# Performance work log

Hardware: AMD Instinct MI355X
Metric: run time of the kernel (lower is better)

Reference implementation:

```python
import jax, jax.numpy as jnp
import numpy as np

IN_F = 1024
OUT_F = 2048
BATCH = 1024
LAMBD = 0.2
TOL = 1e-4
MAX_ITERS = 100


def setup_inputs() -> dict:
    key = jax.random.key(0)
    kx, kw = jax.random.split(key)
    x = jax.random.normal(kx, (BATCH, IN_F), dtype=jnp.float32)
    # weight init exactly as in torch __init__: randn then column-wise (dim=0) L2 normalization
    w = jax.random.normal(kw, (OUT_F, IN_F), dtype=jnp.float32)
    w = w / jnp.linalg.norm(w, axis=0)  # norm over out_features, broadcast over columns
    A = w.T  # (in, out)
    M = A.T @ A + jnp.eye(OUT_F, dtype=jnp.float32)  # (out, out)
    M_inv = jnp.linalg.inv(M).T
    return {"x": x, "weight": w, "M_inv": M_inv}


def _softshrink(z, lambd):
    return jnp.sign(z) * jnp.maximum(jnp.abs(z) - lambd, 0.0)


def _basis_pursuit_admm(A_dot_b, M_inv, lambd=LAMBD, tol=TOL, max_iters=MAX_ITERS):
    # Mask-based equivalent of the torch dynamic-resizing loop: solved rows are
    # frozen instead of removed; v_solution captures v at the iteration a row converges.
    B, Mdim = A_dot_b.shape
    z = jnp.zeros((B, Mdim), dtype=A_dot_b.dtype)
    solved0 = jnp.zeros((B,), dtype=bool)
    init = (z, z, z, z, solved0)  # v, u, v_prev, v_solution, solved

    def step(carry, _):
        v, u, v_prev, v_sol, solved = carry
        b_eff = A_dot_b + v - u                      # (B, M)
        xk = b_eff @ M_inv                           # (B, M) @ (M, M)
        v_new = _softshrink(xk + u, lambd)
        u_new = u + xk - v_new
        # negligible_improvement on the updated v vs previous v
        dx = jnp.linalg.norm(v_new - v_prev, axis=1)
        xn = jnp.linalg.norm(v_new, axis=1)
        conv = (dx / xn) < tol
        newly = conv & (~solved)
        v_sol = jnp.where(newly[:, None], v_new, v_sol)
        frozen = solved[:, None]
        v = jnp.where(frozen, v, v_new)
        u = jnp.where(frozen, u, u_new)
        solved = solved | newly
        return (v, u, v, v_sol, solved), None

    (v, u, v_prev, v_sol, solved), _ = jax.lax.scan(step, init, None, length=max_iters)
    # Matches torch: rows still unsolved after max_iters keep their initial zero solution.
    return v_sol


def reference(x, weight, M_inv):
    input_shape = x.shape
    b = jax.lax.stop_gradient(x.reshape(x.shape[0], -1))  # x.detach() in torch
    A_dot_b = b @ weight.T                                 # b.matmul(A) with A = weight.T
    encoded = _basis_pursuit_admm(A_dot_b, M_inv)
    decoded = encoded @ weight
    return encoded, decoded.reshape(input_shape)
```

## Files before the change

### kernel.cpp

```cpp
#include <hip/hip_runtime.h>
#include <math.h>

#define BATCH 1024
#define IN_F  1024
#define OUT_F 2048
#define LAMBD 0.2f
#define TOL   1e-4f
#define MAX_ITERS 100

#define KSPLIT 4
#define KCHUNK (OUT_F / KSPLIT)
#define BSCALE 32.0f
#define BSCALE_INV 0.03125f

typedef _Float16 half8 __attribute__((ext_vector_type(8)));
typedef _Float16 half4 __attribute__((ext_vector_type(4)));
typedef float    floatx16 __attribute__((ext_vector_type(16)));
typedef unsigned char fp8_t;

#define GLOAD_LDS16(g, l) __builtin_amdgcn_global_load_lds(              \
    (const __attribute__((address_space(1))) void*)(g),                  \
    (__attribute__((address_space(3))) void*)(l), 16, 0, 0)

__device__ inline int pk4_fp8(float a, float b, float c, float d) {
    int w = __builtin_amdgcn_cvt_pk_fp8_f32(a, b, 0, false);
    w = __builtin_amdgcn_cvt_pk_fp8_f32(c, d, w, true);
    return w;
}
__device__ inline fp8_t enc_fp8(float a) {
    return (fp8_t)(__builtin_amdgcn_cvt_pk_fp8_f32(a, a, 0, false) & 0xff);
}
__device__ inline void cvt4_fp8(int w, float o[4]) {
    o[0] = __builtin_amdgcn_cvt_f32_fp8(w, 0);
    o[1] = __builtin_amdgcn_cvt_f32_fp8(w, 1);
    o[2] = __builtin_amdgcn_cvt_f32_fp8(w, 2);
    o[3] = __builtin_amdgcn_cvt_f32_fp8(w, 3);
}

__global__ void init_kernel(float4* __restrict__ v16, float4* __restrict__ u16,
                            float4* __restrict__ enc, int* __restrict__ solved) {
    const int i = blockIdx.x * blockDim.x + threadIdx.x;
    const float4 z = make_float4(0.f, 0.f, 0.f, 0.f);
    const int nh = BATCH * OUT_F / 8;
    const int n4 = BATCH * OUT_F / 4;
    if (i < nh) { v16[i] = z; u16[i] = z; }
    if (i < n4) enc[i] = z;
    if (i < BATCH) solved[i] = 0;
}

__global__ __launch_bounds__(256)
void cast_f16_kernel(const float* __restrict__ in, _Float16* __restrict__ out, int n) {
    const int i = (blockIdx.x * 256 + threadIdx.x) * 4;
    if (i < n) {
        const float4 f = *(const float4*)&in[i];
        half4 h;
        h[0] = (_Float16)f.x; h[1] = (_Float16)f.y;
        h[2] = (_Float16)f.z; h[3] = (_Float16)f.w;
        *(half4*)&out[i] = h;
    }
}

__global__ __launch_bounds__(256)
void transpose_w_kernel(const float* __restrict__ W, _Float16* __restrict__ WT) {
    __shared__ float tile[32][33];
    const int tid = threadIdx.x;
    const int row0 = blockIdx.y * 32;
    const int col0 = blockIdx.x * 32;
    const int r = tid >> 3;
    const int c4 = (tid & 7) * 4;
    const float4 b4 = *(const float4*)&W[(size_t)(row0 + r) * IN_F + col0 + c4];
    tile[r][c4 + 0] = b4.x; tile[r][c4 + 1] = b4.y;
    tile[r][c4 + 2] = b4.z; tile[r][c4 + 3] = b4.w;
    __syncthreads();
    half4 h;
#pragma unroll
    for (int j = 0; j < 4; ++j) h[j] = (_Float16)tile[c4 + j][r];
    *(half4*)&WT[(size_t)(col0 + r) * OUT_F + row0 + c4] = h;
}

__global__ __launch_bounds__(256)
void split_b_kernel(const float* __restrict__ B, fp8_t* __restrict__ BhT) {
    __shared__ float tile[32][33];
    const int tid = threadIdx.x;
    const int k0 = blockIdx.y * 32;
    const int n0 = blockIdx.x * 32;
    const int r = tid >> 3;
    const int c4 = (tid & 7) * 4;
    const float4 b4 = *(const float4*)&B[(size_t)(k0 + r) * OUT_F + n0 + c4];
    tile[r][c4 + 0] = b4.x; tile[r][c4 + 1] = b4.y;
    tile[r][c4 + 2] = b4.z; tile[r][c4 + 3] = b4.w;
    __syncthreads();
    const int w = pk4_fp8(tile[c4 + 0][r] * BSCALE, tile[c4 + 1][r] * BSCALE,
                          tile[c4 + 2][r] * BSCALE, tile[c4 + 3][r] * BSCALE);
    *(int*)&BhT[(size_t)(n0 + r) * OUT_F + k0 + c4] = w;
}

__global__ __launch_bounds__(256)
void mfma_nt_ab(const _Float16* __restrict__ A, const _Float16* __restrict__ B,
                _Float16* __restrict__ Abh, fp8_t* __restrict__ Ah,
                int N, int K) {
    __shared__ _Float16 sA[128 * 32];
    __shared__ _Float16 sB[128 * 32];
    const int tid = threadIdx.x;
    const int m0 = blockIdx.y * 128;
    const int n0 = blockIdx.x * 128;
    const int wv = tid >> 6, ln = tid & 63;
    const int half = ln >> 5, l31 = ln & 31;
    const int wm = (wv >> 1) * 64, wn = (wv & 1) * 64;
    const int r0 = tid >> 2, koff = (tid & 3) * 8;
    const size_t ga0 = (size_t)(m0 + r0) * K + koff;
    const size_t ga1 = (size_t)(m0 + r0 + 64) * K + koff;
    const size_t gb0 = (size_t)(n0 + r0) * K + koff;
    const size_t gb1 = (size_t)(n0 + r0 + 64) * K + koff;
    const int ldst0 = tid * 8, ldst1 = (256 + tid) * 8;

    floatx16 acc[2][2];
#pragma unroll
    for (int a = 0; a < 2; ++a)
#pragma unroll
        for (int b = 0; b < 2; ++b)
#pragma unroll
            for (int q = 0; q < 16; ++q) acc[a][b][q] = 0.f;

    for (int k = 0; k < K; k += 32) {
        __syncthreads();
        GLOAD_LDS16(A + ga0 + k, sA + ldst0);
        GLOAD_LDS16(A + ga1 + k, sA + ldst1);
        GLOAD_LDS16(B + gb0 + k, sB + ldst0);
        GLOAD_LDS16(B + gb1 + k, sB + ldst1);
        __syncthreads();
#pragma unroll
        for (int kk = 0; kk < 2; ++kk) {
            const int ko = kk * 16 + half * 8;
            const half8 a0 = *(const half8*)&sA[(wm + l31) * 32 + ko];
            const half8 a1 = *(const half8*)&sA[(wm + 32 + l31) * 32 + ko];
            const half8 b0 = *(const half8*)&sB[(wn + l31) * 32 + ko];
            const half8 b1 = *(const half8*)&sB[(wn + 32 + l31) * 32 + ko];
            acc[0][0] = __builtin_amdgcn_mfma_f32_32x32x16_f16(a0, b0, acc[0][0], 0, 0, 0);
            acc[0][1] = __builtin_amdgcn_mfma_f32_32x32x16_f16(a0, b1, acc[0][1], 0, 0, 0);
            acc[1][0] = __builtin_amdgcn_mfma_f32_32x32x16_f16(a1, b0, acc[1][0], 0, 0, 0);
            acc[1][1] = __builtin_amdgcn_mfma_f32_32x32x16_f16(a1, b1, acc[1][1], 0, 0, 0);
        }
    }
#pragma unroll
    for (int mm = 0; mm < 2; ++mm)
#pragma unroll
        for (int nn = 0; nn < 2; ++nn) {
            const int col = n0 + wn + nn * 32 + l31;
#pragma unroll
            for (int q = 0; q < 16; ++q) {
                const int row = m0 + wm + mm * 32 + (q & 3) + 8 * (q >> 2) + 4 * half;
                const size_t o = (size_t)row * N + col;
                const float x = acc[mm][nn][q];
                Abh[o] = (_Float16)x;
                Ah[o] = enc_fp8(x);
            }
        }
}

__global__ __launch_bounds__(256)
void mfma_nn_dec(const _Float16* __restrict__ A, const _Float16* __restrict__ B,
                 float* __restrict__ C, int N, int K) {
    __shared__ _Float16 sA[128 * 32];
    __shared__ _Float16 sB[128 * 32];
    const int tid = threadIdx.x;
    const int m0 = blockIdx.y * 128;
    const int n0 = blockIdx.x * 128;
    const int wv = tid >> 6, ln = tid & 63;
    const int half = ln >> 5, l31 = ln & 31;
    const int wm = (wv >> 1) * 64, wn = (wv & 1) * 64;
    const int r0 = tid >> 2, koff = (tid & 3) * 8;
    const size_t ga0 = (size_t)(m0 + r0) * K + koff;
    const size_t ga1 = (size_t)(m0 + r0 + 64) * K + koff;
    const size_t gb0 = (size_t)(n0 + r0) * K + koff;
    const size_t gb1 = (size_t)(n0 + r0 + 64) * K + koff;
    const int ldst0 = tid * 8, ldst1 = (256 + tid) * 8;

    floatx16 acc[2][2];
#pragma unroll
    for (int a = 0; a < 2; ++a)
#pragma unroll
        for (int b = 0; b < 2; ++b)
#pragma unroll
            for (int q = 0; q < 16; ++q) acc[a][b][q] = 0.f;

    for (int k = 0; k < K; k += 32) {
        __syncthreads();
        GLOAD_LDS16(A + ga0 + k, sA + ldst0);
        GLOAD_LDS16(A + ga1 + k, sA + ldst1);
        GLOAD_LDS16(B + gb0 + k, sB + ldst0);
        GLOAD_LDS16(B + gb1 + k, sB + ldst1);
        __syncthreads();
#pragma unroll
        for (int kk = 0; kk < 2; ++kk) {
            const int ko = kk * 16 + half * 8;
            const half8 a0 = *(const half8*)&sA[(wm + l31) * 32 + ko];
            const half8 a1 = *(const half8*)&sA[(wm + 32 + l31) * 32 + ko];
            const half8 b0 = *(const half8*)&sB[(wn + l31) * 32 + ko];
            const half8 b1 = *(const half8*)&sB[(wn + 32 + l31) * 32 + ko];
            acc[0][0] = __builtin_amdgcn_mfma_f32_32x32x16_f16(a0, b0, acc[0][0], 0, 0, 0);
            acc[0][1] = __builtin_amdgcn_mfma_f32_32x32x16_f16(a0, b1, acc[0][1], 0, 0, 0);
            acc[1][0] = __builtin_amdgcn_mfma_f32_32x32x16_f16(a1, b0, acc[1][0], 0, 0, 0);
            acc[1][1] = __builtin_amdgcn_mfma_f32_32x32x16_f16(a1, b1, acc[1][1], 0, 0, 0);
        }
    }
#pragma unroll
    for (int mm = 0; mm < 2; ++mm)
#pragma unroll
        for (int nn = 0; nn < 2; ++nn) {
            const int col = n0 + wn + nn * 32 + l31;
#pragma unroll
            for (int q = 0; q < 16; ++q) {
                const int row = m0 + wm + mm * 32 + (q & 3) + 8 * (q >> 2) + 4 * half;
                C[(size_t)row * N + col] = acc[mm][nn][q];
            }
        }
}

__global__ __launch_bounds__(256)
void xk_mfma(const fp8_t* __restrict__ Ah, const fp8_t* __restrict__ BhT,
             fp8_t* __restrict__ xkp, const int* __restrict__ solved) {
    __shared__ fp8_t smem[16384];
    fp8_t* sA = smem;
    fp8_t* sB = smem + 8192;
    const int tid = threadIdx.x;
    const int m0 = blockIdx.y * 128;
    const int n0 = blockIdx.x * 128;
    const int kz = blockIdx.z;
    constexpr size_t P = (size_t)BATCH * OUT_F;

    __shared__ int s_active;
    if (tid == 0) s_active = 0;
    __syncthreads();
    if (tid < 128 && solved[m0 + tid] == 0) s_active = 1;
    __syncthreads();
    if (!s_active) return;

    const int wv = tid >> 6;
    const int ln = tid & 63;
    const int half = ln >> 5;
    const int l31 = ln & 31;
    const int wm = (wv >> 1) * 64;
    const int wn = (wv & 1) * 64;

    const int r = tid & 127;
    const int c0 = tid >> 7;
    const fp8_t* gA = Ah  + (size_t)(m0 + r) * OUT_F + kz * KCHUNK;
    const fp8_t* gB = BhT + (size_t)(n0 + r) * OUT_F + kz * KCHUNK;
    fp8_t* lA0 = sA + (c0 * 128 + r) * 16;
    fp8_t* lA1 = sA + ((c0 + 2) * 128 + r) * 16;
    fp8_t* lB0 = sB + (c0 * 128 + r) * 16;
    fp8_t* lB1 = sB + ((c0 + 2) * 128 + r) * 16;

    floatx16 acc[2][2];
#pragma unroll
    for (int a = 0; a < 2; ++a)
#pragma unroll
        for (int b = 0; b < 2; ++b)
#pragma unroll
            for (int q = 0; q < 16; ++q) acc[a][b][q] = 0.f;

    const int ao0 = (wm + l31) * 16 + half * 8;
    const int ao1 = (wm + 32 + l31) * 16 + half * 8;
    const int bo0 = (wn + l31) * 16 + half * 8;
    const int bo1 = (wn + 32 + l31) * 16 + half * 8;

    for (int k = 0; k < KCHUNK; k += 64) {
        __syncthreads();
        GLOAD_LDS16(gA + k + c0 * 16, lA0);
        GLOAD_LDS16(gA + k + (c0 + 2) * 16, lA1);
        GLOAD_LDS16(gB + k + c0 * 16, lB0);
        GLOAD_LDS16(gB + k + (c0 + 2) * 16, lB1);
        __syncthreads();

#pragma unroll
        for (int kk = 0; kk < 4; ++kk) {
            const int cb = kk * 2048;
            const long long a0 = *(const long long*)&sA[cb + ao0];
            const long long a1 = *(const long long*)&sA[cb + ao1];
            const long long b0 = *(const long long*)&sB[cb + bo0];
            const long long b1 = *(const long long*)&sB[cb + bo1];
            acc[0][0] = __builtin_amdgcn_mfma_f32_32x32x16_fp8_fp8(a0, b0, acc[0][0], 0, 0, 0);
            acc[0][1] = __builtin_amdgcn_mfma_f32_32x32x16_fp8_fp8(a0, b1, acc[0][1], 0, 0, 0);
            acc[1][0] = __builtin_amdgcn_mfma_f32_32x32x16_fp8_fp8(a1, b0, acc[1][0], 0, 0, 0);
            acc[1][1] = __builtin_amdgcn_mfma_f32_32x32x16_fp8_fp8(a1, b1, acc[1][1], 0, 0, 0);
        }
    }

    __syncthreads();
#pragma unroll
    for (int mm = 0; mm < 2; ++mm)
#pragma unroll
        for (int nn = 0; nn < 2; ++nn) {
            const int lcol = wn + nn * 32 + l31;
#pragma unroll
            for (int q = 0; q < 16; ++q) {
                const int lrow = wm + mm * 32 + (q & 3) + 8 * (q >> 2) + 4 * half;
                smem[lrow * 128 + lcol] = enc_fp8(acc[mm][nn][q] * BSCALE_INV);
            }
        }
    __syncthreads();
    fp8_t* outp = xkp + kz * P + (size_t)m0 * OUT_F + n0;
#pragma unroll
    for (int s = 0; s < 4; ++s) {
        const int f = (s * 256 + tid) * 16;
        *(int4*)&outp[(size_t)(f >> 7) * OUT_F + (f & 127)] = *(const int4*)&smem[f];
    }
}

__global__ __launch_bounds__(256)
void update_kernel(const fp8_t* __restrict__ xkp, const _Float16* __restrict__ Abh,
                   _Float16* __restrict__ v, _Float16* __restrict__ u,
                   float* __restrict__ enc, fp8_t* __restrict__ Ah,
                   int* __restrict__ solved) {
    const int row = blockIdx.x;
    if (solved[row]) return;
    const int t = threadIdx.x;
    constexpr size_t P = (size_t)BATCH * OUT_F;

    const int c = t * 8;
    const size_t off = (size_t)row * OUT_F + c;
    const int2 q0 = *(const int2*)&xkp[off];
    const int2 q1 = *(const int2*)&xkp[P + off];
    const int2 q2 = *(const int2*)&xkp[2 * P + off];
    const int2 q3 = *(const int2*)&xkp[3 * P + off];
    const half8 u8 = *(const half8*)&u[off];
    const half8 v8 = *(const half8*)&v[off];
    const half8 ab8 = *(const half8*)&Abh[off];

    float f0[4], f1[4], f2[4], f3[4], g0[4], g1[4], g2[4], g3[4];
    cvt4_fp8(q0.x, f0); cvt4_fp8(q1.x, f1); cvt4_fp8(q2.x, f2); cvt4_fp8(q3.x, f3);
    cvt4_fp8(q0.y, g0); cvt4_fp8(q1.y, g1); cvt4_fp8(q2.y, g2); cvt4_fp8(q3.y, g3);
    float xs[8];
#pragma unroll
    for (int j = 0; j < 4; ++j) {
        xs[j] = f0[j] + f1[j] + f2[j] + f3[j];
        xs[j + 4] = g0[j] + g1[j] + g2[j] + g3[j];
    }

    float vn_all[8], ae[8];
    half8 vo, uo;
    float dx2 = 0.f, xn2 = 0.f;
#pragma unroll
    for (int j = 0; j < 8; ++j) {
        const float xk = xs[j];
        const float uv = (float)u8[j];
        const float vp = (float)v8[j];
        const float z = xk + uv;
        const float az = fabsf(z) - LAMBD;
        const float vnew = az > 0.f ? copysignf(az, z) : 0.f;
        const float unew = uv + xk - vnew;
        const float d = vnew - vp;
        dx2 += d * d;
        xn2 += vnew * vnew;
        vn_all[j] = vnew;
        vo[j] = (_Float16)vnew;
        uo[j] = (_Float16)unew;
        ae[j] = (float)ab8[j] + vnew - unew;
    }
    *(half8*)&v[off] = vo;
    *(half8*)&u[off] = uo;
    int2 ah;
    ah.x = pk4_fp8(ae[0], ae[1], ae[2], ae[3]);
    ah.y = pk4_fp8(ae[4], ae[5], ae[6], ae[7]);
    *(int2*)&Ah[off] = ah;

#pragma unroll
    for (int o = 32; o > 0; o >>= 1) {
        dx2 += __shfl_down(dx2, o);
        xn2 += __shfl_down(xn2, o);
    }
    __shared__ float sdx[4], sxn[4];
    __shared__ float s_conv;
    if ((t & 63) == 0) { sdx[t >> 6] = dx2; sxn[t >> 6] = xn2; }
    __syncthreads();
    if (t == 0) {
        const float dxt = sqrtf(sdx[0] + sdx[1] + sdx[2] + sdx[3]);
        const float xnt = sqrtf(sxn[0] + sxn[1] + sxn[2] + sxn[3]);
        const bool conv = (dxt / xnt) < TOL;
        s_conv = conv ? 1.f : 0.f;
        if (conv) solved[row] = 1;
    }
    __syncthreads();
    if (s_conv != 0.f) {
        *(float4*)&enc[off] = make_float4(vn_all[0], vn_all[1], vn_all[2], vn_all[3]);
        *(float4*)&enc[off + 4] = make_float4(vn_all[4], vn_all[5], vn_all[6], vn_all[7]);
    }
}

extern "C" void kernel_launch(void* const* d_in, const int* in_sizes, int n_in,
                              void* d_out, int out_size, void* d_ws, size_t ws_size,
                              hipStream_t stream) {
    (void)in_sizes; (void)n_in; (void)out_size; (void)ws_size;
    const float* x    = (const float*)d_in[0];
    const float* w    = (const float*)d_in[1];
    const float* Minv = (const float*)d_in[2];

    float* enc = (float*)d_out;
    float* dec = enc + (size_t)BATCH * OUT_F;

    constexpr size_t P = (size_t)BATCH * OUT_F;
    _Float16* Abh = (_Float16*)d_ws;
    _Float16* v   = Abh + P;
    _Float16* u   = v + P;
    _Float16* xh  = u + P;
    _Float16* wh  = xh + (size_t)BATCH * IN_F;
    _Float16* whT = wh + (size_t)OUT_F * IN_F;
    _Float16* ench = whT + (size_t)IN_F * OUT_F;
    fp8_t* Ah  = (fp8_t*)(ench + P);
    fp8_t* xkp = Ah + P;
    fp8_t* BhT = xkp + 4 * P;
    int* solved = (int*)(BhT + (size_t)OUT_F * OUT_F);

    {
        const int n = BATCH * OUT_F / 4;
        init_kernel<<<(n + 255) / 256, 256, 0, stream>>>(
            (float4*)v, (float4*)u, (float4*)enc, solved);
    }

    split_b_kernel<<<dim3(OUT_F / 32, OUT_F / 32), 256, 0, stream>>>(Minv, BhT);

    cast_f16_kernel<<<(BATCH * IN_F / 4 + 255) / 256, 256, 0, stream>>>(x, xh, BATCH * IN_F);
    cast_f16_kernel<<<(OUT_F * IN_F / 4 + 255) / 256, 256, 0, stream>>>(w, wh, OUT_F * IN_F);
    transpose_w_kernel<<<dim3(IN_F / 32, OUT_F / 32), 256, 0, stream>>>(w, whT);

    mfma_nt_ab<<<dim3(OUT_F / 128, BATCH / 128), 256, 0, stream>>>(
        xh, wh, Abh, Ah, OUT_F, IN_F);

    for (int it = 0; it < MAX_ITERS; ++it) {
        xk_mfma<<<dim3(OUT_F / 128, BATCH / 128, KSPLIT), 256, 0, stream>>>(
            Ah, BhT, xkp, solved);
        update_kernel<<<BATCH, 256, 0, stream>>>(xkp, Abh, v, u, enc, Ah, solved);
    }

    cast_f16_kernel<<<(BATCH * OUT_F / 4 + 255) / 256, 256, 0, stream>>>(enc, ench, BATCH * OUT_F);
    mfma_nn_dec<<<dim3(IN_F / 128, BATCH / 128), 256, 0, stream>>>(
        ench, whT, dec, IN_F, OUT_F);
}
```

Measured before the change: 2.282 ms.

## Fuse ADMM update into split-K GEMM kernel with tile-level counter synchronization

Merges the per-iteration elementwise update into the xk GEMM kernel. Each block first applies the previous iteration's update on its own tile, then spin-waits on per-tile atomic counters before running the next GEMM, so the separate update launch disappears and update work overlaps with GEMM work from other blocks. The convergence check becomes deferred: per-tile partial norms are double-buffered, and a row is frozen one iteration later using its stored v. xk partials are double-buffered as well. The cost is extra buffers, spin-waiting that depends on all blocks being co-resident, and more complex bookkeeping for solved rows.

```diff
diff --git a/kernel.cpp b/kernel.cpp
--- a/kernel.cpp
+++ b/kernel.cpp
@@ -38,14 +38,16 @@
 }
 
 __global__ void init_kernel(float4* __restrict__ v16, float4* __restrict__ u16,
-                            float4* __restrict__ enc, int* __restrict__ solved) {
+                            float4* __restrict__ enc, int* __restrict__ solved,
+                            int* __restrict__ cnt) {
     const int i = blockIdx.x * blockDim.x + threadIdx.x;
     const float4 z = make_float4(0.f, 0.f, 0.f, 0.f);
     const int nh = BATCH * OUT_F / 8;
     const int n4 = BATCH * OUT_F / 4;
     if (i < nh) { v16[i] = z; u16[i] = z; }
     if (i < n4) enc[i] = z;
-    if (i < BATCH) solved[i] = 0;
+    if (i < BATCH) solved[i] = -1;
+    if (i < 128) cnt[i] = 0;
 }
 
 __global__ __launch_bounds__(256)
@@ -217,27 +219,148 @@
         }
 }
 
-__global__ __launch_bounds__(256)
-void xk_mfma(const fp8_t* __restrict__ Ah, const fp8_t* __restrict__ BhT,
-             fp8_t* __restrict__ xkp, const int* __restrict__ solved) {
+__global__ __launch_bounds__(256, 2)
+void admm_step(int d, int do_gemm,
+               const fp8_t* __restrict__ BhT, fp8_t* __restrict__ Ah,
+               fp8_t* __restrict__ xkp_w, const fp8_t* __restrict__ xkp_r,
+               const _Float16* __restrict__ Abh, _Float16* __restrict__ v,
+               _Float16* __restrict__ u, float* __restrict__ enc,
+               int* __restrict__ solved, int* __restrict__ cnt,
+               float* __restrict__ pdx_w, float* __restrict__ pxn_w,
+               const float* __restrict__ pdx_r, const float* __restrict__ pxn_r) {
     __shared__ fp8_t smem[16384];
     fp8_t* sA = smem;
     fp8_t* sB = smem + 8192;
+    __shared__ int s_active;
+    constexpr size_t P = (size_t)BATCH * OUT_F;
+
     const int tid = threadIdx.x;
-    const int m0 = blockIdx.y * 128;
-    const int n0 = blockIdx.x * 128;
-    const int kz = blockIdx.z;
-    constexpr size_t P = (size_t)BATCH * OUT_F;
-
-    __shared__ int s_active;
+    const int bid = blockIdx.x;
+    const int ni = bid & 15, mi = (bid >> 4) & 7, kz = bid >> 7;
+    const int m0 = mi * 128, n0 = ni * 128;
+    const int ln = tid & 63;
+
+    if (d >= 1) {
+        const int t = d - 1;
+        const int row = m0 + kz * 32 + (tid >> 3);
+        const int co = n0 + (tid & 7) * 16;
+        const size_t off = (size_t)row * OUT_F + co;
+
+        const int s = solved[row];
+        bool conv = false;
+        if (t >= 1) {
+            float sd = 0.f, sn = 0.f;
+            if ((tid & 7) == 0) {
+#pragma unroll
+                for (int q = 0; q < 16; ++q) {
+                    sd += pdx_r[q * BATCH + row];
+                    sn += pxn_r[q * BATCH + row];
+                }
+            }
+            const int base = ln & ~7;
+            sd = __shfl(sd, base);
+            sn = __shfl(sn, base);
+            conv = (sqrtf(sd) / sqrtf(sn)) < TOL;
+        }
+        const bool newly = conv && (s == -1 || s == t - 1);
+        if (newly) {
+            if ((tid & 7) == 0) solved[row] = t - 1;
+            const half8 va = *(const half8*)&v[off];
+            const half8 vb = *(const half8*)&v[off + 8];
+            float4 e0, e1, e2, e3;
+            e0 = make_float4((float)va[0], (float)va[1], (float)va[2], (float)va[3]);
+            e1 = make_float4((float)va[4], (float)va[5], (float)va[6], (float)va[7]);
+            e2 = make_float4((float)vb[0], (float)vb[1], (float)vb[2], (float)vb[3]);
+            e3 = make_float4((float)vb[4], (float)vb[5], (float)vb[6], (float)vb[7]);
+            *(float4*)&enc[off] = e0;  *(float4*)&enc[off + 4] = e1;
+            *(float4*)&enc[off + 8] = e2; *(float4*)&enc[off + 12] = e3;
+        }
+        const bool frozen = (s != -1) || newly;
+        if (!frozen) {
+            const int4 q0 = *(const int4*)&xkp_r[off];
+            const int4 q1 = *(const int4*)&xkp_r[P + off];
+            const int4 q2 = *(const int4*)&xkp_r[2 * P + off];
+            const int4 q3 = *(const int4*)&xkp_r[3 * P + off];
+            const half8 va = *(const half8*)&v[off];
+            const half8 vb = *(const half8*)&v[off + 8];
+            const half8 ua = *(const half8*)&u[off];
+            const half8 ub = *(const half8*)&u[off + 8];
+            const half8 aa = *(const half8*)&Abh[off];
+            const half8 ab = *(const half8*)&Abh[off + 8];
+            const int w0[4] = {q0.x, q0.y, q0.z, q0.w};
+            const int w1[4] = {q1.x, q1.y, q1.z, q1.w};
+            const int w2[4] = {q2.x, q2.y, q2.z, q2.w};
+            const int w3[4] = {q3.x, q3.y, q3.z, q3.w};
+            half8 vo[2], uo[2];
+            int aw[4];
+            float dx2 = 0.f, xn2 = 0.f;
+#pragma unroll
+            for (int g = 0; g < 4; ++g) {
+                float a0[4], a1[4], a2[4], a3[4], ae4[4];
+                cvt4_fp8(w0[g], a0); cvt4_fp8(w1[g], a1);
+                cvt4_fp8(w2[g], a2); cvt4_fp8(w3[g], a3);
+#pragma unroll
+                for (int j = 0; j < 4; ++j) {
+                    const int idx = g * 4 + j;
+                    const float xk = a0[j] + a1[j] + a2[j] + a3[j];
+                    const float uv = (float)((idx < 8) ? ua[idx] : ub[idx - 8]);
+                    const float vp = (float)((idx < 8) ? va[idx] : vb[idx - 8]);
+                    const float z = xk + uv;
+                    const float az = fabsf(z) - LAMBD;
+                    const float vnew = az > 0.f ? copysignf(az, z) : 0.f;
+                    const float unew = uv + xk - vnew;
+                    const float dd = vnew - vp;
+                    dx2 += dd * dd;
+                    xn2 += vnew * vnew;
+                    if (idx < 8) { vo[0][idx] = (_Float16)vnew; uo[0][idx] = (_Float16)unew; }
+                    else { vo[1][idx - 8] = (_Float16)vnew; uo[1][idx - 8] = (_Float16)unew; }
+                    ae4[j] = (float)((idx < 8) ? aa[idx] : ab[idx - 8]) + vnew - unew;
+                }
+                aw[g] = pk4_fp8(ae4[0], ae4[1], ae4[2], ae4[3]);
+            }
+            *(half8*)&v[off] = vo[0]; *(half8*)&v[off + 8] = vo[1];
+            *(half8*)&u[off] = uo[0]; *(half8*)&u[off + 8] = uo[1];
+            *(int4*)&Ah[off] = make_int4(aw[0], aw[1], aw[2], aw[3]);
+            dx2 += __shfl_xor(dx2, 1); dx2 += __shfl_xor(dx2, 2); dx2 += __shfl_xor(dx2, 4);
+            xn2 += __shfl_xor(xn2, 1); xn2 += __shfl_xor(xn2, 2); xn2 += __shfl_xor(xn2, 4);
+            if ((tid & 7) == 0) {
+                pdx_w[ni * BATCH + row] = dx2;
+                pxn_w[ni * BATCH + row] = xn2;
+            }
+        }
+        __syncthreads();
+        if (tid == 0) {
+            __threadfence();
+            __hip_atomic_fetch_add(&cnt[mi * 16 + ni], 1,
+                                   __ATOMIC_RELEASE, __HIP_MEMORY_SCOPE_AGENT);
+        }
+    }
+
+    if (!do_gemm) return;
+
+    if (d >= 1) {
+        if (tid == 0) {
+            const int target = 4 * d;
+#pragma unroll
+            for (int q = 0; q < 4; ++q) {
+                int* f = &cnt[mi * 16 + kz * 4 + q];
+                while (__hip_atomic_load(f, __ATOMIC_RELAXED,
+                                         __HIP_MEMORY_SCOPE_AGENT) < target) {
+                    __builtin_amdgcn_s_sleep(4);
+                }
+            }
+            __threadfence();
+        }
+        __syncthreads();
+    }
+
     if (tid == 0) s_active = 0;
     __syncthreads();
-    if (tid < 128 && solved[m0 + tid] == 0) s_active = 1;
+    if (tid < 128 && solved[m0 + tid] == -1) s_active = 1;
     __syncthreads();
     if (!s_active) return;
 
     const int wv = tid >> 6;
-    const int ln = tid & 63;
     const int half = ln >> 5;
     const int l31 = ln & 31;
     const int wm = (wv >> 1) * 64;
@@ -272,7 +395,6 @@
         GLOAD_LDS16(gB + k + c0 * 16, lB0);
         GLOAD_LDS16(gB + k + (c0 + 2) * 16, lB1);
         __syncthreads();
-
 #pragma unroll
         for (int kk = 0; kk < 4; ++kk) {
             const int cb = kk * 2048;
@@ -300,7 +422,7 @@
             }
         }
     __syncthreads();
-    fp8_t* outp = xkp + kz * P + (size_t)m0 * OUT_F + n0;
+    fp8_t* outp = xkp_w + (size_t)kz * P + (size_t)m0 * OUT_F + n0;
 #pragma unroll
     for (int s = 0; s < 4; ++s) {
         const int f = (s * 256 + tid) * 16;
@@ -309,82 +431,29 @@
 }
 
 __global__ __launch_bounds__(256)
-void update_kernel(const fp8_t* __restrict__ xkp, const _Float16* __restrict__ Abh,
-                   _Float16* __restrict__ v, _Float16* __restrict__ u,
-                   float* __restrict__ enc, fp8_t* __restrict__ Ah,
-                   int* __restrict__ solved) {
+void final_conv(const float* __restrict__ pdx, const float* __restrict__ pxn,
+                const _Float16* __restrict__ v, const int* __restrict__ solved,
+                float* __restrict__ enc) {
     const int row = blockIdx.x;
-    if (solved[row]) return;
-    const int t = threadIdx.x;
-    constexpr size_t P = (size_t)BATCH * OUT_F;
-
-    const int c = t * 8;
-    const size_t off = (size_t)row * OUT_F + c;
-    const int2 q0 = *(const int2*)&xkp[off];
-    const int2 q1 = *(const int2*)&xkp[P + off];
-    const int2 q2 = *(const int2*)&xkp[2 * P + off];
-    const int2 q3 = *(const int2*)&xkp[3 * P + off];
-    const half8 u8 = *(const half8*)&u[off];
-    const half8 v8 = *(const half8*)&v[off];
-    const half8 ab8 = *(const half8*)&Abh[off];
-
-    float f0[4], f1[4], f2[4], f3[4], g0[4], g1[4], g2[4], g3[4];
-    cvt4_fp8(q0.x, f0); cvt4_fp8(q1.x, f1); cvt4_fp8(q2.x, f2); cvt4_fp8(q3.x, f3);
-    cvt4_fp8(q0.y, g0); cvt4_fp8(q1.y, g1); cvt4_fp8(q2.y, g2); cvt4_fp8(q3.y, g3);
-    float xs[8];
-#pragma unroll
-    for (int j = 0; j < 4; ++j) {
-        xs[j] = f0[j] + f1[j] + f2[j] + f3[j];
-        xs[j + 4] = g0[j] + g1[j] + g2[j] + g3[j];
-    }
-
-    float vn_all[8], ae[8];
-    half8 vo, uo;
-    float dx2 = 0.f, xn2 = 0.f;
-#pragma unroll
-    for (int j = 0; j < 8; ++j) {
-        const float xk = xs[j];
-        const float uv = (float)u8[j];
-        const float vp = (float)v8[j];
-        const float z = xk + uv;
-        const float az = fabsf(z) - LAMBD;
-        const float vnew = az > 0.f ? copysignf(az, z) : 0.f;
-        const float unew = uv + xk - vnew;
-        const float d = vnew - vp;
-        dx2 += d * d;
-        xn2 += vnew * vnew;
-        vn_all[j] = vnew;
-        vo[j] = (_Float16)vnew;
-        uo[j] = (_Float16)unew;
-        ae[j] = (float)ab8[j] + vnew - unew;
-    }
-    *(half8*)&v[off] = vo;
-    *(half8*)&u[off] = uo;
-    int2 ah;
-    ah.x = pk4_fp8(ae[0], ae[1], ae[2], ae[3]);
-    ah.y = pk4_fp8(ae[4], ae[5], ae[6], ae[7]);
-    *(int2*)&Ah[off] = ah;
-
-#pragma unroll
-    for (int o = 32; o > 0; o >>= 1) {
-        dx2 += __shfl_down(dx2, o);
-        xn2 += __shfl_down(xn2, o);
-    }
-    __shared__ float sdx[4], sxn[4];
-    __shared__ float s_conv;
-    if ((t & 63) == 0) { sdx[t >> 6] = dx2; sxn[t >> 6] = xn2; }
-    __syncthreads();
-    if (t == 0) {
-        const float dxt = sqrtf(sdx[0] + sdx[1] + sdx[2] + sdx[3]);
-        const float xnt = sqrtf(sxn[0] + sxn[1] + sxn[2] + sxn[3]);
-        const bool conv = (dxt / xnt) < TOL;
-        s_conv = conv ? 1.f : 0.f;
-        if (conv) solved[row] = 1;
-    }
-    __syncthreads();
-    if (s_conv != 0.f) {
-        *(float4*)&enc[off] = make_float4(vn_all[0], vn_all[1], vn_all[2], vn_all[3]);
-        *(float4*)&enc[off + 4] = make_float4(vn_all[4], vn_all[5], vn_all[6], vn_all[7]);
+    __shared__ float ssd, ssn;
+    if (threadIdx.x == 0) {
+        float sd = 0.f, sn = 0.f;
+        for (int q = 0; q < 16; ++q) {
+            sd += pdx[q * BATCH + row];
+            sn += pxn[q * BATCH + row];
+        }
+        ssd = sd; ssn = sn;
+    }
+    __syncthreads();
+    if (solved[row] == -1 && (sqrtf(ssd) / sqrtf(ssn)) < TOL) {
+        const size_t base = (size_t)row * OUT_F;
+        for (int c = threadIdx.x * 8; c < OUT_F; c += 2048) {
+            const half8 vv = *(const half8*)&v[base + c];
+            *(float4*)&enc[base + c] =
+                make_float4((float)vv[0], (float)vv[1], (float)vv[2], (float)vv[3]);
+            *(float4*)&enc[base + c + 4] =
+                make_float4((float)vv[4], (float)vv[5], (float)vv[6], (float)vv[7]);
+        }
     }
 }
 
@@ -406,33 +475,52 @@
     _Float16* xh  = u + P;
     _Float16* wh  = xh + (size_t)BATCH * IN_F;
     _Float16* whT = wh + (size_t)OUT_F * IN_F;
-    _Float16* ench = whT + (size_t)IN_F * OUT_F;
-    fp8_t* Ah  = (fp8_t*)(ench + P);
-    fp8_t* xkp = Ah + P;
-    fp8_t* BhT = xkp + 4 * P;
-    int* solved = (int*)(BhT + (size_t)OUT_F * OUT_F);
+    fp8_t* Ah   = (fp8_t*)(whT + (size_t)IN_F * OUT_F);
+    fp8_t* xkpA = Ah + P;
+    fp8_t* xkpB = xkpA + 4 * P;
+    fp8_t* BhT  = xkpB + 4 * P;
+    float* pdx0 = (float*)(BhT + (size_t)OUT_F * OUT_F);
+    float* pxn0 = pdx0 + 16 * BATCH;
+    float* pdx1 = pxn0 + 16 * BATCH;
+    float* pxn1 = pdx1 + 16 * BATCH;
+    int* solved = (int*)(pxn1 + 16 * BATCH);
+    int* cnt = solved + BATCH;
 
     {
         const int n = BATCH * OUT_F / 4;
         init_kernel<<<(n + 255) / 256, 256, 0, stream>>>(
-            (float4*)v, (float4*)u, (float4*)enc, solved);
+            (float4*)v, (float4*)u, (float4*)enc, solved, cnt);
     }
 
     split_b_kernel<<<dim3(OUT_F / 32, OUT_F / 32), 256, 0, stream>>>(Minv, BhT);
-
     cast_f16_kernel<<<(BATCH * IN_F / 4 + 255) / 256, 256, 0, stream>>>(x, xh, BATCH * IN_F);
-    cast_f16_kernel<<<(OUT_F * IN_F / 4 + 255) / 256, 256, 0, stream>>>(w, wh, OUT_F * IN_F);
     transpose_w_kernel<<<dim3(IN_F / 32, OUT_F / 32), 256, 0, stream>>>(w, whT);
+    cast_f16_kernel<<<(OUT_F * IN_F / 4 + 255) / 256, 256, 0, stream>>>(w, wh + 0, OUT_F * IN_F);
 
     mfma_nt_ab<<<dim3(OUT_F / 128, BATCH / 128), 256, 0, stream>>>(
         xh, wh, Abh, Ah, OUT_F, IN_F);
 
-    for (int it = 0; it < MAX_ITERS; ++it) {
-        xk_mfma<<<dim3(OUT_F / 128, BATCH / 128, KSPLIT), 256, 0, stream>>>(
-            Ah, BhT, xkp, solved);
-        update_kernel<<<BATCH, 256, 0, stream>>>(xkp, Abh, v, u, enc, Ah, solved);
-    }
-
+    for (int d = 0; d < MAX_ITERS; ++d) {
+        fp8_t* xw = (d & 1) ? xkpB : xkpA;
+        fp8_t* xr = (d & 1) ? xkpA : xkpB;
+        const int t = d - 1;
+        float* pw_dx = (t >= 0 && (t & 1)) ? pdx1 : pdx0;
+        float* pw_xn = (t >= 0 && (t & 1)) ? pxn1 : pxn0;
+        const float* pr_dx = (t >= 1 && ((t - 1) & 1)) ? pdx1 : pdx0;
+        const float* pr_xn = (t >= 1 && ((t - 1) & 1)) ? pxn1 : pxn0;
+        admm_step<<<512, 256, 0, stream>>>(d, 1, BhT, Ah, xw, xr, Abh, v, u, enc,
+                                           solved, cnt, pw_dx, pw_xn, pr_dx, pr_xn);
+    }
+    {
+        const int d = MAX_ITERS;
+        fp8_t* xw = (d & 1) ? xkpB : xkpA;
+        fp8_t* xr = (d & 1) ? xkpA : xkpB;
+        admm_step<<<512, 256, 0, stream>>>(d, 0, BhT, Ah, xw, xr, Abh, v, u, enc,
+                                           solved, cnt, pdx1, pxn1, pdx0, pxn0);
+    }
+    final_conv<<<BATCH, 256, 0, stream>>>(pdx1, pxn1, v, solved, enc);
+
+    _Float16* ench = wh;
     cast_f16_kernel<<<(BATCH * OUT_F / 4 + 255) / 256, 256, 0, stream>>>(enc, ench, BATCH * OUT_F);
     mfma_nn_dec<<<dim3(IN_F / 128, BATCH / 128), 256, 0, stream>>>(
         ench, whT, dec, IN_F, OUT_F);
```

Measured after the change: 6.886 ms. 3.02x slower.

## Halve xk GEMM row tile and store A_dot_b as fp8

Applied to the files above, without the earlier changes.

The iterative xk GEMM kernel now uses 64x128 output tiles instead of 128x128. This doubles the number of blocks and lets early-exit skipping act on 64-row groups of solved batch rows. A_dot_b is stored once as fp8 rather than fp16, which reduces the bytes read per ADMM update. In exchange, each block gets less operand reuse, and the fp8 A_dot_b loses precision in the b_eff term.

```diff
diff --git a/kernel.cpp b/kernel.cpp
--- a/kernel.cpp
+++ b/kernel.cpp
@@ -97,7 +97,7 @@
 
 __global__ __launch_bounds__(256)
 void mfma_nt_ab(const _Float16* __restrict__ A, const _Float16* __restrict__ B,
-                _Float16* __restrict__ Abh, fp8_t* __restrict__ Ah,
+                fp8_t* __restrict__ Ab8, fp8_t* __restrict__ Ah,
                 int N, int K) {
     __shared__ _Float16 sA[128 * 32];
     __shared__ _Float16 sB[128 * 32];
@@ -151,9 +151,9 @@
             for (int q = 0; q < 16; ++q) {
                 const int row = m0 + wm + mm * 32 + (q & 3) + 8 * (q >> 2) + 4 * half;
                 const size_t o = (size_t)row * N + col;
-                const float x = acc[mm][nn][q];
-                Abh[o] = (_Float16)x;
-                Ah[o] = enc_fp8(x);
+                const fp8_t e = enc_fp8(acc[mm][nn][q]);
+                Ab8[o] = e;
+                Ah[o] = e;
             }
         }
 }
@@ -220,11 +220,10 @@
 __global__ __launch_bounds__(256)
 void xk_mfma(const fp8_t* __restrict__ Ah, const fp8_t* __restrict__ BhT,
              fp8_t* __restrict__ xkp, const int* __restrict__ solved) {
-    __shared__ fp8_t smem[16384];
-    fp8_t* sA = smem;
-    fp8_t* sB = smem + 8192;
+    __shared__ fp8_t sA[64 * 64];
+    __shared__ fp8_t sB[128 * 64];
     const int tid = threadIdx.x;
-    const int m0 = blockIdx.y * 128;
+    const int m0 = blockIdx.y * 64;
     const int n0 = blockIdx.x * 128;
     const int kz = blockIdx.z;
     constexpr size_t P = (size_t)BATCH * OUT_F;
@@ -232,84 +231,66 @@
     __shared__ int s_active;
     if (tid == 0) s_active = 0;
     __syncthreads();
-    if (tid < 128 && solved[m0 + tid] == 0) s_active = 1;
+    if (tid < 64 && solved[m0 + tid] == 0) s_active = 1;
     __syncthreads();
     if (!s_active) return;
 
-    const int wv = tid >> 6;
-    const int ln = tid & 63;
-    const int half = ln >> 5;
-    const int l31 = ln & 31;
-    const int wm = (wv >> 1) * 64;
+    const int wv = tid >> 6, ln = tid & 63;
+    const int half = ln >> 5, l31 = ln & 31;
+    const int wm = (wv >> 1) * 32;
     const int wn = (wv & 1) * 64;
 
-    const int r = tid & 127;
-    const int c0 = tid >> 7;
-    const fp8_t* gA = Ah  + (size_t)(m0 + r) * OUT_F + kz * KCHUNK;
-    const fp8_t* gB = BhT + (size_t)(n0 + r) * OUT_F + kz * KCHUNK;
-    fp8_t* lA0 = sA + (c0 * 128 + r) * 16;
-    fp8_t* lA1 = sA + ((c0 + 2) * 128 + r) * 16;
-    fp8_t* lB0 = sB + (c0 * 128 + r) * 16;
-    fp8_t* lB1 = sB + ((c0 + 2) * 128 + r) * 16;
-
-    floatx16 acc[2][2];
-#pragma unroll
-    for (int a = 0; a < 2; ++a)
-#pragma unroll
-        for (int b = 0; b < 2; ++b)
-#pragma unroll
-            for (int q = 0; q < 16; ++q) acc[a][b][q] = 0.f;
-
-    const int ao0 = (wm + l31) * 16 + half * 8;
-    const int ao1 = (wm + 32 + l31) * 16 + half * 8;
-    const int bo0 = (wn + l31) * 16 + half * 8;
-    const int bo1 = (wn + 32 + l31) * 16 + half * 8;
+    const int ar = tid & 63, ac = tid >> 6;
+    const fp8_t* gA = Ah + (size_t)(m0 + ar) * OUT_F + kz * KCHUNK + ac * 16;
+    fp8_t* lA = sA + (ac * 64 + ar) * 16;
+    const int br = tid & 127, bc0 = tid >> 7;
+    const fp8_t* gB = BhT + (size_t)(n0 + br) * OUT_F + kz * KCHUNK;
+    fp8_t* lB0 = sB + (bc0 * 128 + br) * 16;
+    fp8_t* lB1 = sB + ((bc0 + 2) * 128 + br) * 16;
+
+    floatx16 acc[2];
+#pragma unroll
+    for (int b = 0; b < 2; ++b)
+#pragma unroll
+        for (int q = 0; q < 16; ++q) acc[b][q] = 0.f;
 
     for (int k = 0; k < KCHUNK; k += 64) {
         __syncthreads();
-        GLOAD_LDS16(gA + k + c0 * 16, lA0);
-        GLOAD_LDS16(gA + k + (c0 + 2) * 16, lA1);
-        GLOAD_LDS16(gB + k + c0 * 16, lB0);
-        GLOAD_LDS16(gB + k + (c0 + 2) * 16, lB1);
-        __syncthreads();
-
+        GLOAD_LDS16(gA + k, lA);
+        GLOAD_LDS16(gB + k + bc0 * 16, lB0);
+        GLOAD_LDS16(gB + k + (bc0 + 2) * 16, lB1);
+        __syncthreads();
 #pragma unroll
         for (int kk = 0; kk < 4; ++kk) {
-            const int cb = kk * 2048;
-            const long long a0 = *(const long long*)&sA[cb + ao0];
-            const long long a1 = *(const long long*)&sA[cb + ao1];
-            const long long b0 = *(const long long*)&sB[cb + bo0];
-            const long long b1 = *(const long long*)&sB[cb + bo1];
-            acc[0][0] = __builtin_amdgcn_mfma_f32_32x32x16_fp8_fp8(a0, b0, acc[0][0], 0, 0, 0);
-            acc[0][1] = __builtin_amdgcn_mfma_f32_32x32x16_fp8_fp8(a0, b1, acc[0][1], 0, 0, 0);
-            acc[1][0] = __builtin_amdgcn_mfma_f32_32x32x16_fp8_fp8(a1, b0, acc[1][0], 0, 0, 0);
-            acc[1][1] = __builtin_amdgcn_mfma_f32_32x32x16_fp8_fp8(a1, b1, acc[1][1], 0, 0, 0);
-        }
-    }
-
-    __syncthreads();
-#pragma unroll
-    for (int mm = 0; mm < 2; ++mm)
-#pragma unroll
-        for (int nn = 0; nn < 2; ++nn) {
-            const int lcol = wn + nn * 32 + l31;
-#pragma unroll
-            for (int q = 0; q < 16; ++q) {
-                const int lrow = wm + mm * 32 + (q & 3) + 8 * (q >> 2) + 4 * half;
-                smem[lrow * 128 + lcol] = enc_fp8(acc[mm][nn][q] * BSCALE_INV);
-            }
-        }
-    __syncthreads();
-    fp8_t* outp = xkp + kz * P + (size_t)m0 * OUT_F + n0;
-#pragma unroll
-    for (int s = 0; s < 4; ++s) {
+            const long long a0 = *(const long long*)&sA[(kk * 64 + wm + l31) * 16 + half * 8];
+            const long long b0 = *(const long long*)&sB[(kk * 128 + wn + l31) * 16 + half * 8];
+            const long long b1 = *(const long long*)&sB[(kk * 128 + wn + 32 + l31) * 16 + half * 8];
+            acc[0] = __builtin_amdgcn_mfma_f32_32x32x16_fp8_fp8(a0, b0, acc[0], 0, 0, 0);
+            acc[1] = __builtin_amdgcn_mfma_f32_32x32x16_fp8_fp8(a0, b1, acc[1], 0, 0, 0);
+        }
+    }
+
+    __syncthreads();
+#pragma unroll
+    for (int nn = 0; nn < 2; ++nn) {
+        const int lcol = wn + nn * 32 + l31;
+#pragma unroll
+        for (int q = 0; q < 16; ++q) {
+            const int lrow = wm + (q & 3) + 8 * (q >> 2) + 4 * half;
+            sB[lrow * 128 + lcol] = enc_fp8(acc[nn][q] * BSCALE_INV);
+        }
+    }
+    __syncthreads();
+    fp8_t* outp = xkp + (size_t)kz * P + (size_t)m0 * OUT_F + n0;
+#pragma unroll
+    for (int s = 0; s < 2; ++s) {
         const int f = (s * 256 + tid) * 16;
-        *(int4*)&outp[(size_t)(f >> 7) * OUT_F + (f & 127)] = *(const int4*)&smem[f];
-    }
-}
-
-__global__ __launch_bounds__(256)
-void update_kernel(const fp8_t* __restrict__ xkp, const _Float16* __restrict__ Abh,
+        *(int4*)&outp[(size_t)(f >> 7) * OUT_F + (f & 127)] = *(const int4*)&sB[f];
+    }
+}
+
+__global__ __launch_bounds__(256)
+void update_kernel(const fp8_t* __restrict__ xkp, const fp8_t* __restrict__ Ab8,
                    _Float16* __restrict__ v, _Float16* __restrict__ u,
                    float* __restrict__ enc, fp8_t* __restrict__ Ah,
                    int* __restrict__ solved) {
@@ -326,16 +307,20 @@
     const int2 q3 = *(const int2*)&xkp[3 * P + off];
     const half8 u8 = *(const half8*)&u[off];
     const half8 v8 = *(const half8*)&v[off];
-    const half8 ab8 = *(const half8*)&Abh[off];
+    const int2 ab2 = *(const int2*)&Ab8[off];
 
     float f0[4], f1[4], f2[4], f3[4], g0[4], g1[4], g2[4], g3[4];
     cvt4_fp8(q0.x, f0); cvt4_fp8(q1.x, f1); cvt4_fp8(q2.x, f2); cvt4_fp8(q3.x, f3);
     cvt4_fp8(q0.y, g0); cvt4_fp8(q1.y, g1); cvt4_fp8(q2.y, g2); cvt4_fp8(q3.y, g3);
-    float xs[8];
+    float ab0[4], ab1[4];
+    cvt4_fp8(ab2.x, ab0); cvt4_fp8(ab2.y, ab1);
+    float xs[8], abv[8];
 #pragma unroll
     for (int j = 0; j < 4; ++j) {
         xs[j] = f0[j] + f1[j] + f2[j] + f3[j];
         xs[j + 4] = g0[j] + g1[j] + g2[j] + g3[j];
+        abv[j] = ab0[j];
+        abv[j + 4] = ab1[j];
     }
 
     float vn_all[8], ae[8];
@@ -356,7 +341,7 @@
         vn_all[j] = vnew;
         vo[j] = (_Float16)vnew;
         uo[j] = (_Float16)unew;
-        ae[j] = (float)ab8[j] + vnew - unew;
+        ae[j] = abv[j] + vnew - unew;
     }
     *(half8*)&v[off] = vo;
     *(half8*)&u[off] = uo;
@@ -400,8 +385,8 @@
     float* dec = enc + (size_t)BATCH * OUT_F;
 
     constexpr size_t P = (size_t)BATCH * OUT_F;
-    _Float16* Abh = (_Float16*)d_ws;
-    _Float16* v   = Abh + P;
+    fp8_t* Ab8 = (fp8_t*)d_ws;
+    _Float16* v   = (_Float16*)(Ab8 + P);
     _Float16* u   = v + P;
     _Float16* xh  = u + P;
     _Float16* wh  = xh + (size_t)BATCH * IN_F;
@@ -425,12 +410,12 @@
     transpose_w_kernel<<<dim3(IN_F / 32, OUT_F / 32), 256, 0, stream>>>(w, whT);
 
     mfma_nt_ab<<<dim3(OUT_F / 128, BATCH / 128), 256, 0, stream>>>(
-        xh, wh, Abh, Ah, OUT_F, IN_F);
+        xh, wh, Ab8, Ah, OUT_F, IN_F);
 
     for (int it = 0; it < MAX_ITERS; ++it) {
-        xk_mfma<<<dim3(OUT_F / 128, BATCH / 128, KSPLIT), 256, 0, stream>>>(
+        xk_mfma<<<dim3(OUT_F / 128, BATCH / 64, KSPLIT), 256, 0, stream>>>(
             Ah, BhT, xkp, solved);
-        update_kernel<<<BATCH, 256, 0, stream>>>(xkp, Abh, v, u, enc, Ah, solved);
+        update_kernel<<<BATCH, 256, 0, stream>>>(xkp, Ab8, v, u, enc, Ah, solved);
     }
 
     cast_f16_kernel<<<(BATCH * OUT_F / 4 + 255) / 256, 256, 0, stream>>>(enc, ench, BATCH * OUT_F);
```

New measurement: 2.608 ms. 14.3% more time.
